# Kernel optimization log

Measured on AMD Instinct MI355X. Metric: run time of the kernel, lower is better.

The kernel has to match this reference:

```python
import jax, jax.numpy as jnp
import numpy as np

N_ELEC = 8192   # electrons (nodes)
N_NUC = 512     # nuclei
EMB = 256       # embedding_dim
KER = 256       # kernel_dim
DF = 64         # dist_feat_dim
MID = 128       # round(sqrt(DF*KER)), log-interpolated hidden width of w-MLP
E = 131072      # edges per edge type


def _ssp(x):
    # shifted softplus, deepqmc default activation: log(0.5*exp(x) + 0.5)
    return jax.nn.softplus(x) - jnp.log(2.0)


def setup_inputs() -> dict:
    key = jax.random.key(0)
    ks = jax.random.split(key, 24)
    def nrm(k, shape, scale):
        return jax.random.normal(k, shape, dtype=jnp.float32) * scale
    inp = {}
    inp['electrons'] = nrm(ks[0], (N_ELEC, EMB), 1.0)
    inp['nuclei'] = nrm(ks[1], (N_NUC, KER), 1.0)
    for i, lbl in enumerate(['same', 'anti', 'n']):
        inp[f'dist_{lbl}'] = jax.random.uniform(ks[2 + i], (E, DF), dtype=jnp.float32)
        inp[f'w1_{lbl}'] = nrm(ks[5 + i], (DF, MID), DF ** -0.5)
        inp[f'b1_{lbl}'] = jnp.zeros((MID,), jnp.float32)
        inp[f'w2_{lbl}'] = nrm(ks[8 + i], (MID, KER), MID ** -0.5)
        inp[f'g_{lbl}'] = nrm(ks[11 + i], (KER, EMB), KER ** -0.5)
    inp['h_w'] = nrm(ks[14], (EMB, KER), EMB ** -0.5)
    inp['senders_same'] = jax.random.randint(ks[15], (E,), 0, N_ELEC)
    inp['senders_anti'] = jax.random.randint(ks[16], (E,), 0, N_ELEC)
    inp['senders_n'] = jax.random.randint(ks[17], (E,), 0, N_NUC)
    inp['receivers_same'] = jax.random.randint(ks[18], (E,), 0, N_ELEC)
    inp['receivers_anti'] = jax.random.randint(ks[19], (E,), 0, N_ELEC)
    inp['receivers_n'] = jax.random.randint(ks[20], (E,), 0, N_ELEC)
    return inp


def reference(electrons, nuclei, dist_same, dist_anti, dist_n,
              w1_same, b1_same, w2_same, w1_anti, b1_anti, w2_anti,
              w1_n, b1_n, w2_n, g_same, g_anti, g_n, h_w,
              senders_same, senders_anti, senders_n,
              receivers_same, receivers_anti, receivers_n):
    def w_mlp(d, w1, b1, w2):
        # MLP with ('log', 2) hidden layers: linear+bias -> SSP -> last linear (no bias)
        return _ssp(d @ w1 + b1) @ w2

    # per-edge filters from distance features: [E, KER]
    we_same = w_mlp(dist_same, w1_same, b1_same, w2_same)
    we_anti = w_mlp(dist_anti, w1_anti, b1_anti, w2_anti)
    we_n = w_mlp(dist_n, w1_n, b1_n, w2_n)

    # shared h (single bias-free linear) on gathered sender electrons: [E, KER]
    hx_same = electrons[senders_same] @ h_w
    hx_anti = electrons[senders_anti] @ h_w

    weh_same = we_same * hx_same
    weh_anti = we_anti * hx_anti
    weh_n = we_n * nuclei[senders_n]

    # scatter-sum messages to receiver electrons: [N_ELEC, KER]
    z_same = jax.ops.segment_sum(weh_same, receivers_same, num_segments=N_ELEC)
    z_anti = jax.ops.segment_sum(weh_anti, receivers_anti, num_segments=N_ELEC)
    z_n = jax.ops.segment_sum(weh_n, receivers_n, num_segments=N_ELEC)

    # per-label g (single bias-free linear) + residual update, order matches original
    return electrons + (z_n @ g_n + z_same @ g_same + z_anti @ g_anti)
```

## Files before the change

kernel.cpp:

```cpp
#include <hip/hip_runtime.h>
#include <stdint.h>


#define N_ELEC 8192
#define N_NUC  512
#define EMB    256
#define KER    256
#define DF     64
#define MID    128
#define NEDGE  131072
#define RPS    8256
#define CSTR   272

using u16 = unsigned short;
typedef short short8 __attribute__((ext_vector_type(8)));
typedef float f32x4 __attribute__((ext_vector_type(4)));

__device__ __forceinline__ float bf2f(u16 h) {
  return __uint_as_float(((unsigned)h) << 16);
}
__device__ __forceinline__ u16 f2bf(float f) {
  unsigned u = __float_as_uint(f);
  return (u16)((u + 0x7FFFu + ((u >> 16) & 1u)) >> 16);
}
__device__ __forceinline__ unsigned pkbf(float a, float b) {
  return ((unsigned)f2bf(b) << 16) | (unsigned)f2bf(a);
}
__device__ __forceinline__ float ssp_fast(float x) {
  const float e = __expf(-fabsf(x));
  return fmaxf(x, 0.f) + __logf(fmaf(0.5f, e, 0.5f));
}

__device__ __forceinline__ void bar_lds() {
  __builtin_amdgcn_sched_barrier(0);
  asm volatile("s_waitcnt lgkmcnt(0)" ::: "memory");
  __builtin_amdgcn_s_barrier();
  __builtin_amdgcn_sched_barrier(0);
}

__device__ __forceinline__ void stage_t64(const char* g0, long stride,
                                          char* lds, int tid) {
  const int l = tid & 63, w = tid >> 6;
  const int r = w * 16 + (l >> 2);
  const int cb = (l & 3) * 16;
  __builtin_amdgcn_global_load_lds(
      (const __attribute__((address_space(1))) unsigned*)(g0 +
                                                          (long)r * stride +
                                                          cb),
      (__attribute__((address_space(3))) unsigned*)(lds + w * 1024), 16, 0, 0);
}
__device__ __forceinline__ void stage_f64(const float* g0, int stride_e,
                                          int kt, char* lds, int tid) {
#pragma unroll
  for (int k = 0; k < 4; ++k) {
    const int idx2 = k * 256 + tid;
    const int row = idx2 >> 4, cp = idx2 & 15;
    const float2 v = *(const float2*)(g0 + (long)row * stride_e + kt + cp * 2);
    *(unsigned*)(lds + row * 64 + cp * 4) = pkbf(v.x, v.y);
  }
}
template <bool A_F32>
__device__ __forceinline__ void gemm64(const char* A0, long as_bytes,
                                       const float* Af, int as_elems,
                                       const char* B0, long bs, int K,
                                       char* As, char* Bs, f32x4 acc[2][2],
                                       int tid) {
  const int l = tid & 63, lane15 = l & 15, quad = l >> 4, wv = tid >> 6;
  const int mw = (wv >> 1) * 32, nw = (wv & 1) * 32;
  for (int kt = 0; kt < K; kt += 32) {
    if (A_F32)
      stage_f64(Af, as_elems, kt, As, tid);
    else
      stage_t64(A0 + (long)kt * 2, as_bytes, As, tid);
    stage_t64(B0 + (long)kt * 2, bs, Bs, tid);
    __syncthreads();
    short8 af[2], bf[2];
#pragma unroll
    for (int i = 0; i < 2; ++i) {
      af[i] = *(const short8*)(As + (mw + i * 16 + lane15) * 64 + quad * 16);
      bf[i] = *(const short8*)(Bs + (nw + i * 16 + lane15) * 64 + quad * 16);
    }
#pragma unroll
    for (int mi = 0; mi < 2; ++mi)
#pragma unroll
      for (int ni = 0; ni < 2; ++ni)
        acc[mi][ni] = __builtin_amdgcn_mfma_f32_16x16x32_bf16(
            af[mi], bf[ni], acc[mi][ni], 0, 0, 0);
    __syncthreads();
  }
}

__global__ __launch_bounds__(256) void k_setup(
    const float* h_w, const float* w1s, const float* w1a, const float* w1n,
    const float* w2s, const float* w2a, const float* w2n, const float* gs,
    const float* ga, const float* gn, u16* hwT, u16* w1T, u16* w2T, u16* gT,
    float4* z, int* cnt) {
  const int b = blockIdx.x;
  if (b < 6144) {
    z[b * 256 + threadIdx.x] = (float4){0.f, 0.f, 0.f, 0.f};
    return;
  }
  if (b < 6240) {
    cnt[(b - 6144) * 256 + threadIdx.x] = 0;
    return;
  }
  int i = (b - 6240) * 256 + threadIdx.x;
  if (i < 65536) {
    int n = i >> 8, k = i & 255;
    hwT[i] = f2bf(h_w[k * 256 + n]);
    return;
  }
  int j = i - 65536;
  if (j < 24576) {
    int t = j >> 13, jj = j & 8191, n = jj >> 6, k = jj & 63;
    const float* w1 = t == 0 ? w1s : (t == 1 ? w1a : w1n);
    w1T[j] = f2bf(w1[k * 128 + n]);
    return;
  }
  j -= 24576;
  if (j < 98304) {
    int t = j >> 15, jj = j & 32767, n = jj >> 7, k = jj & 127;
    const float* w2 = t == 0 ? w2s : (t == 1 ? w2a : w2n);
    w2T[j] = f2bf(w2[k * 256 + n]);
    return;
  }
  j -= 98304;
  if (j < 196608) {
    int n = j / 768, q = j % 768, t = q >> 8, k = q & 255;
    const float* g = t == 0 ? gs : (t == 1 ? ga : gn);
    gT[j] = f2bf(g[k * 256 + n]);
  }
}

__global__ __launch_bounds__(256) void k_hist(const int* r0, const int* r1,
                                              const int* r2, int* cnt) {
  const int t = blockIdx.z;
  const int* rcv = t == 0 ? r0 : (t == 1 ? r1 : r2);
  const int e = blockIdx.x * 256 + threadIdx.x;
  atomicAdd(&cnt[t * N_ELEC + rcv[e]], 1);
}

__global__ __launch_bounds__(256) void k_scan(const int* cnt, int* rowptr,
                                              int* cursor) {
  const int t = blockIdx.x, tid = threadIdx.x;
  __shared__ int part[256];
  const int* c = cnt + t * N_ELEC;
  int s = 0;
#pragma unroll
  for (int i = 0; i < 32; ++i) s += c[tid * 32 + i];
  part[tid] = s;
  __syncthreads();
  for (int off = 1; off < 256; off <<= 1) {
    int v = (tid >= off) ? part[tid - off] : 0;
    __syncthreads();
    part[tid] += v;
    __syncthreads();
  }
  int run = (tid == 0) ? 0 : part[tid - 1];
  int* rp = rowptr + t * RPS;
  int* cu = cursor + t * N_ELEC;
  for (int i = 0; i < 32; ++i) {
    rp[tid * 32 + i] = run;
    cu[tid * 32 + i] = run;
    run += c[tid * 32 + i];
  }
  if (tid == 255) rp[N_ELEC] = run;
}

__global__ __launch_bounds__(256) void k_place(const int* r0, const int* r1,
                                               const int* r2, const int* s0,
                                               const int* s1, const int* s2,
                                               int* cursor, int* perm,
                                               int* snd_s, int* rcv_s) {
  const int t = blockIdx.z;
  const int* rcv = t == 0 ? r0 : (t == 1 ? r1 : r2);
  const int* snd = t == 0 ? s0 : (t == 1 ? s1 : s2);
  const int e = blockIdx.x * 256 + threadIdx.x;
  const int rr = rcv[e];
  const int pos = atomicAdd(&cursor[t * N_ELEC + rr], 1);
  perm[t * NEDGE + pos] = e;
  snd_s[t * NEDGE + pos] = snd[e];
  rcv_s[t * NEDGE + pos] = rr;
}

__global__ __launch_bounds__(256) void k_he(const float* elec, const u16* hwT,
                                            u16* he) {
  __shared__ char As[4096], Bs[4096];
  f32x4 acc[2][2];
#pragma unroll
  for (int i = 0; i < 2; ++i)
#pragma unroll
    for (int j = 0; j < 2; ++j) acc[i][j] = (f32x4){0.f, 0.f, 0.f, 0.f};
  const int m0 = blockIdx.x * 64, n0 = blockIdx.y * 64;
  gemm64<true>(nullptr, 0, elec + (long)m0 * 256, 256,
               (const char*)hwT + (long)n0 * 512, 512, 256, As, Bs, acc,
               threadIdx.x);
  const int l = threadIdx.x & 63, lane15 = l & 15, quad = l >> 4,
            wv = threadIdx.x >> 6;
  const int mw = (wv >> 1) * 32, nw = (wv & 1) * 32;
#pragma unroll
  for (int mi = 0; mi < 2; ++mi)
#pragma unroll
    for (int r = 0; r < 4; ++r) {
      const int row = m0 + mw + mi * 16 + quad * 4 + r;
#pragma unroll
      for (int ni = 0; ni < 2; ++ni) {
        const int col = n0 + nw + ni * 16 + lane15;
        he[row * 256 + col] = f2bf(acc[mi][ni][r]);
      }
    }
}

__global__ __launch_bounds__(256, 3) void k_edge(
    const float* d0, const float* d1, const float* d2, const float* b0,
    const float* b1p, const float* b2, const u16* w1T, const u16* w2T,
    const u16* he, const float* nucf, const int* perm, const int* snd_s,
    const int* rcv_s, float* z) {
  __shared__ char mid[128 * CSTR];
  __shared__ char hc[64 * CSTR];
  __shared__ int snd_l[128], rcv_l[128];

  const int t = blockIdx.z;
  const int m0 = blockIdx.x * 128;
  const int tid = threadIdx.x;
  const float* dist = t == 0 ? d0 : (t == 1 ? d1 : d2);
  const float* bias = t == 0 ? b0 : (t == 1 ? b1p : b2);
  const u16* w1t = w1T + t * 8192;
  const u16* w2t = w2T + t * 32768;
  const bool is_nuc = (t == 2);

  if (tid < 128)
    snd_l[tid] = snd_s[t * NEDGE + m0 + tid];
  else
    rcv_l[tid - 128] = rcv_s[t * NEDGE + m0 + tid - 128];

  int rows[4];
  const int* pm = perm + t * NEDGE + m0;
#pragma unroll
  for (int s = 0; s < 4; ++s) rows[s] = pm[(s * 256 + tid) >> 3];
#pragma unroll
  for (int j = 0; j < 2; ++j)
#pragma unroll
    for (int s = 0; s < 4; ++s) {
      const int idx = s * 256 + tid, row = idx >> 3, ch = idx & 7;
      const float4 v =
          *(const float4*)(dist + (long)rows[s] * 64 + j * 32 + ch * 4);
      uint2 p;
      p.x = pkbf(v.x, v.y);
      p.y = pkbf(v.z, v.w);
      *(uint2*)(mid + j * 8192 + row * 64 + ch * 8) = p;
    }
  bar_lds();

  const int l = tid & 63, lane15 = l & 15, quad = l >> 4, wv = tid >> 6;
  const int mw = (wv >> 1) * 64, nw = (wv & 1) * 64;

  f32x4 acc[4][4];
#pragma unroll
  for (int i = 0; i < 4; ++i)
#pragma unroll
    for (int j = 0; j < 4; ++j) acc[i][j] = (f32x4){0.f, 0.f, 0.f, 0.f};
#pragma unroll
  for (int j = 0; j < 2; ++j) {
    short8 af[4], bf[4];
#pragma unroll
    for (int i = 0; i < 4; ++i) {
      af[i] = *(const short8*)(mid + j * 8192 + (mw + i * 16 + lane15) * 64 +
                               quad * 16);
      bf[i] = *(const short8*)(w1t + (nw + i * 16 + lane15) * 64 + j * 32 +
                               quad * 8);
    }
#pragma unroll
    for (int mi = 0; mi < 4; ++mi)
#pragma unroll
      for (int ni = 0; ni < 4; ++ni)
        acc[mi][ni] = __builtin_amdgcn_mfma_f32_16x16x32_bf16(
            af[mi], bf[ni], acc[mi][ni], 0, 0, 0);
  }
  bar_lds();

#pragma unroll
  for (int mi = 0; mi < 4; ++mi)
#pragma unroll
    for (int r = 0; r < 4; ++r) {
      const int row = mw + mi * 16 + quad * 4 + r;
#pragma unroll
      for (int ni = 0; ni < 4; ++ni) {
        const int col = nw + ni * 16 + lane15;
        const float x = acc[mi][ni][r] + bias[col];
        *(u16*)(mid + row * CSTR + col * 2) = f2bf(ssp_fast(x));
      }
    }
  bar_lds();

  for (int n0 = 0; n0 < 256; n0 += 128) {
#pragma unroll
    for (int i = 0; i < 4; ++i)
#pragma unroll
      for (int j = 0; j < 4; ++j) acc[i][j] = (f32x4){0.f, 0.f, 0.f, 0.f};
#pragma unroll
    for (int kt = 0; kt < 128; kt += 32) {
      short8 af[4], bf[4];
#pragma unroll
      for (int i = 0; i < 4; ++i) {
        af[i] = *(const short8*)(mid + (mw + i * 16 + lane15) * CSTR + kt * 2 +
                                 quad * 16);
        bf[i] = *(const short8*)(w2t + (n0 + nw + i * 16 + lane15) * 128 + kt +
                                 quad * 8);
      }
#pragma unroll
      for (int mi = 0; mi < 4; ++mi)
#pragma unroll
        for (int ni = 0; ni < 4; ++ni)
          acc[mi][ni] = __builtin_amdgcn_mfma_f32_16x16x32_bf16(
              af[mi], bf[ni], acc[mi][ni], 0, 0, 0);
    }

    for (int h = 0; h < 2; ++h) {
      const int rbase = h * 64;
      if (!is_nuc) {
#pragma unroll
        for (int c = 0; c < 4; ++c) {
          const int chunk = c * 256 + tid;
          const int row = chunk >> 4, off = chunk & 15;
          const uint4 v =
              *(const uint4*)((const char*)he +
                              (size_t)snd_l[rbase + row] * 512 + n0 * 2 +
                              off * 16);
          *(uint4*)(hc + row * CSTR + off * 16) = v;
        }
      } else {
#pragma unroll
        for (int c = 0; c < 4; ++c) {
          const int chunk = c * 256 + tid;
          const int row = chunk >> 4, off = chunk & 15;
          const char* src = (const char*)nucf +
                            (size_t)snd_l[rbase + row] * 1024 + n0 * 4 +
                            off * 32;
          const float4 a = *(const float4*)src;
          const float4 b = *(const float4*)(src + 16);
          uint4 p;
          p.x = pkbf(a.x, a.y);
          p.y = pkbf(a.z, a.w);
          p.z = pkbf(b.x, b.y);
          p.w = pkbf(b.z, b.w);
          *(uint4*)(hc + row * CSTR + off * 16) = p;
        }
      }
      bar_lds();

      if ((wv >> 1) == h) {
#pragma unroll
        for (int mi = 0; mi < 4; ++mi)
#pragma unroll
          for (int r = 0; r < 4; ++r) {
            const int lrow = mi * 16 + quad * 4 + r;
#pragma unroll
            for (int ni = 0; ni < 4; ++ni) {
              const int col = nw + ni * 16 + lane15;
              u16* p = (u16*)(hc + lrow * CSTR) + col;
              *p = f2bf(acc[mi][ni][r] * bf2f(*p));
            }
          }
      }
      bar_lds();

      {
        const int cp = l;
        const int rbeg = wv * 16, rend = rbeg + 16;
        float a0 = 0.f, a1 = 0.f;
        int cur = rcv_l[rbase + rbeg];
        for (int row = rbeg; row < rend; ++row) {
          const unsigned p = *(const unsigned*)(hc + row * CSTR + cp * 4);
          a0 += __uint_as_float(p << 16);
          a1 += __uint_as_float(p & 0xffff0000u);
          const int nxt = (row + 1 < rend) ? rcv_l[rbase + row + 1] : -1;
          if (nxt != cur) {
            float* zp = z + (size_t)cur * 768 + t * 256 + n0 + cp * 2;
            unsafeAtomicAdd(zp, a0);
            unsafeAtomicAdd(zp + 1, a1);
            a0 = a1 = 0.f;
            cur = nxt;
          }
        }
      }
      bar_lds();
    }
  }
}

__global__ __launch_bounds__(256) void k_final(const float* z, const u16* gT,
                                               const float* elec, float* out) {
  __shared__ char As[4096], Bs[4096];
  f32x4 acc[2][2];
#pragma unroll
  for (int i = 0; i < 2; ++i)
#pragma unroll
    for (int j = 0; j < 2; ++j) acc[i][j] = (f32x4){0.f, 0.f, 0.f, 0.f};
  const int m0 = blockIdx.x * 64, n0 = blockIdx.y * 64;
  gemm64<true>(nullptr, 0, z + (long)m0 * 768, 768,
               (const char*)gT + (long)n0 * 1536, 1536, 768, As, Bs, acc,
               threadIdx.x);
  const int l = threadIdx.x & 63, lane15 = l & 15, quad = l >> 4,
            wv = threadIdx.x >> 6;
  const int mw = (wv >> 1) * 32, nw = (wv & 1) * 32;
#pragma unroll
  for (int mi = 0; mi < 2; ++mi)
#pragma unroll
    for (int r = 0; r < 4; ++r) {
      const int row = m0 + mw + mi * 16 + quad * 4 + r;
#pragma unroll
      for (int ni = 0; ni < 2; ++ni) {
        const int col = n0 + nw + ni * 16 + lane15;
        out[row * 256 + col] = acc[mi][ni][r] + elec[row * 256 + col];
      }
    }
}

extern "C" void kernel_launch(void* const* d_in, const int* in_sizes, int n_in,
                              void* d_out, int out_size, void* d_ws,
                              size_t ws_size, hipStream_t stream) {
  int I_dist[3], I_w1[3], I_b1[3], I_w2[3], I_g[3], I_hw;
  if (in_sizes[3] == 64 * 128) {
    for (int t = 0; t < 3; ++t) {
      I_dist[t] = 2 + t * 5 + 0;
      I_w1[t] = 2 + t * 5 + 1;
      I_b1[t] = 2 + t * 5 + 2;
      I_w2[t] = 2 + t * 5 + 3;
      I_g[t] = 2 + t * 5 + 4;
    }
    I_hw = 17;
  } else {
    I_dist[0] = 2; I_dist[1] = 3; I_dist[2] = 4;
    I_w1[0] = 5;  I_b1[0] = 6;  I_w2[0] = 7;
    I_w1[1] = 8;  I_b1[1] = 9;  I_w2[1] = 10;
    I_w1[2] = 11; I_b1[2] = 12; I_w2[2] = 13;
    I_g[0] = 14; I_g[1] = 15; I_g[2] = 16;
    I_hw = 17;
  }
  const int I_snd[3] = {18, 19, 20};
  const int I_rcv[3] = {21, 22, 23};

  char* ws = (char*)d_ws;
  u16* he = (u16*)(ws + 0);
  u16* hwT = (u16*)(ws + 4194304);
  u16* w1T = (u16*)(ws + 4325376);
  u16* w2T = (u16*)(ws + 4374528);
  u16* gT = (u16*)(ws + 4571136);
  float* z = (float*)(ws + 4964352);
  int* cnt = (int*)(ws + 30130176);
  int* rowptr = (int*)(ws + 30228480);
  int* cursor = (int*)(ws + 30327552);
  int* perm = (int*)(ws + 30425856);
  int* snd_s = (int*)(ws + 31998720);
  int* rcv_s = (int*)(ws + 33571584);

  const float* elec = (const float*)d_in[0];
  const float* nuc = (const float*)d_in[1];
  const int* s0 = (const int*)d_in[I_snd[0]];
  const int* s1 = (const int*)d_in[I_snd[1]];
  const int* s2 = (const int*)d_in[I_snd[2]];
  const int* r0 = (const int*)d_in[I_rcv[0]];
  const int* r1 = (const int*)d_in[I_rcv[1]];
  const int* r2 = (const int*)d_in[I_rcv[2]];

  k_setup<<<7744, 256, 0, stream>>>(
      (const float*)d_in[I_hw], (const float*)d_in[I_w1[0]],
      (const float*)d_in[I_w1[1]], (const float*)d_in[I_w1[2]],
      (const float*)d_in[I_w2[0]], (const float*)d_in[I_w2[1]],
      (const float*)d_in[I_w2[2]], (const float*)d_in[I_g[0]],
      (const float*)d_in[I_g[1]], (const float*)d_in[I_g[2]], hwT, w1T, w2T,
      gT, (float4*)z, cnt);

  k_hist<<<dim3(NEDGE / 256, 1, 3), 256, 0, stream>>>(r0, r1, r2, cnt);
  k_scan<<<3, 256, 0, stream>>>(cnt, rowptr, cursor);
  k_place<<<dim3(NEDGE / 256, 1, 3), 256, 0, stream>>>(r0, r1, r2, s0, s1, s2,
                                                       cursor, perm, snd_s,
                                                       rcv_s);

  k_he<<<dim3(N_ELEC / 64, 4), 256, 0, stream>>>(elec, hwT, he);

  k_edge<<<dim3(NEDGE / 128, 1, 3), 256, 0, stream>>>(
      (const float*)d_in[I_dist[0]], (const float*)d_in[I_dist[1]],
      (const float*)d_in[I_dist[2]], (const float*)d_in[I_b1[0]],
      (const float*)d_in[I_b1[1]], (const float*)d_in[I_b1[2]], w1T, w2T, he,
      nuc, perm, snd_s, rcv_s, z);

  k_final<<<dim3(N_ELEC / 64, 4), 256, 0, stream>>>(z, gT, elec,
                                                    (float*)d_out);
}
```

Measured before the change: 403.4 us.

## Pack sorted edge metadata into u64 and double k_edge threads to 512

```diff
diff --git a/kernel.cpp b/kernel.cpp
--- a/kernel.cpp
+++ b/kernel.cpp
@@ -13,6 +13,7 @@
 #define CSTR   272
 
 using u16 = unsigned short;
+using u64 = unsigned long long;
 typedef short short8 __attribute__((ext_vector_type(8)));
 typedef float f32x4 __attribute__((ext_vector_type(4)));
 
@@ -170,17 +171,15 @@
 __global__ __launch_bounds__(256) void k_place(const int* r0, const int* r1,
                                                const int* r2, const int* s0,
                                                const int* s1, const int* s2,
-                                               int* cursor, int* perm,
-                                               int* snd_s, int* rcv_s) {
+                                               int* cursor, u64* pk) {
   const int t = blockIdx.z;
   const int* rcv = t == 0 ? r0 : (t == 1 ? r1 : r2);
   const int* snd = t == 0 ? s0 : (t == 1 ? s1 : s2);
   const int e = blockIdx.x * 256 + threadIdx.x;
   const int rr = rcv[e];
   const int pos = atomicAdd(&cursor[t * N_ELEC + rr], 1);
-  perm[t * NEDGE + pos] = e;
-  snd_s[t * NEDGE + pos] = snd[e];
-  rcv_s[t * NEDGE + pos] = rr;
+  pk[t * NEDGE + pos] =
+      (u64)(unsigned)e | ((u64)(unsigned)snd[e] << 17) | ((u64)(unsigned)rr << 30);
 }
 
 __global__ __launch_bounds__(256) void k_he(const float* elec, const u16* hwT,
@@ -211,11 +210,10 @@
     }
 }
 
-__global__ __launch_bounds__(256, 3) void k_edge(
+__global__ __launch_bounds__(512, 6) void k_edge(
     const float* d0, const float* d1, const float* d2, const float* b0,
     const float* b1p, const float* b2, const u16* w1T, const u16* w2T,
-    const u16* he, const float* nucf, const int* perm, const int* snd_s,
-    const int* rcv_s, float* z) {
+    const u16* he, const float* nucf, const u64* pk, float* z) {
   __shared__ char mid[128 * CSTR];
   __shared__ char hc[64 * CSTR];
   __shared__ int snd_l[128], rcv_l[128];
@@ -228,21 +226,23 @@
   const u16* w1t = w1T + t * 8192;
   const u16* w2t = w2T + t * 32768;
   const bool is_nuc = (t == 2);
-
-  if (tid < 128)
-    snd_l[tid] = snd_s[t * NEDGE + m0 + tid];
-  else
-    rcv_l[tid - 128] = rcv_s[t * NEDGE + m0 + tid - 128];
-
-  int rows[4];
-  const int* pm = perm + t * NEDGE + m0;
-#pragma unroll
-  for (int s = 0; s < 4; ++s) rows[s] = pm[(s * 256 + tid) >> 3];
+  const u64* pkt = pk + (size_t)t * NEDGE + m0;
+
+  if (tid < 128) {
+    const u64 rec = pkt[tid];
+    snd_l[tid] = (int)((rec >> 17) & 0x1FFFu);
+    rcv_l[tid] = (int)(rec >> 30);
+  }
+
+  int rows[2];
+#pragma unroll
+  for (int s = 0; s < 2; ++s)
+    rows[s] = (int)(pkt[(s * 512 + tid) >> 3] & 0x1FFFFu);
 #pragma unroll
   for (int j = 0; j < 2; ++j)
 #pragma unroll
-    for (int s = 0; s < 4; ++s) {
-      const int idx = s * 256 + tid, row = idx >> 3, ch = idx & 7;
+    for (int s = 0; s < 2; ++s) {
+      const int idx = s * 512 + tid, row = idx >> 3, ch = idx & 7;
       const float4 v =
           *(const float4*)(dist + (long)rows[s] * 64 + j * 32 + ch * 4);
       uint2 p;
@@ -253,27 +253,30 @@
   bar_lds();
 
   const int l = tid & 63, lane15 = l & 15, quad = l >> 4, wv = tid >> 6;
-  const int mw = (wv >> 1) * 64, nw = (wv & 1) * 64;
-
-  f32x4 acc[4][4];
+  const int mwh = wv >> 2;
+  const int mw = mwh * 64;
+  const int nw = (wv & 3) * 32;
+
+  f32x4 acc[4][2];
 #pragma unroll
   for (int i = 0; i < 4; ++i)
 #pragma unroll
-    for (int j = 0; j < 4; ++j) acc[i][j] = (f32x4){0.f, 0.f, 0.f, 0.f};
+    for (int j = 0; j < 2; ++j) acc[i][j] = (f32x4){0.f, 0.f, 0.f, 0.f};
 #pragma unroll
   for (int j = 0; j < 2; ++j) {
-    short8 af[4], bf[4];
-#pragma unroll
-    for (int i = 0; i < 4; ++i) {
+    short8 af[4], bf[2];
+#pragma unroll
+    for (int i = 0; i < 4; ++i)
       af[i] = *(const short8*)(mid + j * 8192 + (mw + i * 16 + lane15) * 64 +
                                quad * 16);
+#pragma unroll
+    for (int i = 0; i < 2; ++i)
       bf[i] = *(const short8*)(w1t + (nw + i * 16 + lane15) * 64 + j * 32 +
                                quad * 8);
-    }
 #pragma unroll
     for (int mi = 0; mi < 4; ++mi)
 #pragma unroll
-      for (int ni = 0; ni < 4; ++ni)
+      for (int ni = 0; ni < 2; ++ni)
         acc[mi][ni] = __builtin_amdgcn_mfma_f32_16x16x32_bf16(
             af[mi], bf[ni], acc[mi][ni], 0, 0, 0);
   }
@@ -285,7 +288,7 @@
     for (int r = 0; r < 4; ++r) {
       const int row = mw + mi * 16 + quad * 4 + r;
 #pragma unroll
-      for (int ni = 0; ni < 4; ++ni) {
+      for (int ni = 0; ni < 2; ++ni) {
         const int col = nw + ni * 16 + lane15;
         const float x = acc[mi][ni][r] + bias[col];
         *(u16*)(mid + row * CSTR + col * 2) = f2bf(ssp_fast(x));
@@ -297,21 +300,22 @@
 #pragma unroll
     for (int i = 0; i < 4; ++i)
 #pragma unroll
-      for (int j = 0; j < 4; ++j) acc[i][j] = (f32x4){0.f, 0.f, 0.f, 0.f};
+      for (int j = 0; j < 2; ++j) acc[i][j] = (f32x4){0.f, 0.f, 0.f, 0.f};
 #pragma unroll
     for (int kt = 0; kt < 128; kt += 32) {
-      short8 af[4], bf[4];
-#pragma unroll
-      for (int i = 0; i < 4; ++i) {
+      short8 af[4], bf[2];
+#pragma unroll
+      for (int i = 0; i < 4; ++i)
         af[i] = *(const short8*)(mid + (mw + i * 16 + lane15) * CSTR + kt * 2 +
                                  quad * 16);
+#pragma unroll
+      for (int i = 0; i < 2; ++i)
         bf[i] = *(const short8*)(w2t + (n0 + nw + i * 16 + lane15) * 128 + kt +
                                  quad * 8);
-      }
 #pragma unroll
       for (int mi = 0; mi < 4; ++mi)
 #pragma unroll
-        for (int ni = 0; ni < 4; ++ni)
+        for (int ni = 0; ni < 2; ++ni)
           acc[mi][ni] = __builtin_amdgcn_mfma_f32_16x16x32_bf16(
               af[mi], bf[ni], acc[mi][ni], 0, 0, 0);
     }
@@ -320,8 +324,8 @@
       const int rbase = h * 64;
       if (!is_nuc) {
 #pragma unroll
-        for (int c = 0; c < 4; ++c) {
-          const int chunk = c * 256 + tid;
+        for (int c = 0; c < 2; ++c) {
+          const int chunk = c * 512 + tid;
           const int row = chunk >> 4, off = chunk & 15;
           const uint4 v =
               *(const uint4*)((const char*)he +
@@ -331,8 +335,8 @@
         }
       } else {
 #pragma unroll
-        for (int c = 0; c < 4; ++c) {
-          const int chunk = c * 256 + tid;
+        for (int c = 0; c < 2; ++c) {
+          const int chunk = c * 512 + tid;
           const int row = chunk >> 4, off = chunk & 15;
           const char* src = (const char*)nucf +
                             (size_t)snd_l[rbase + row] * 1024 + n0 * 4 +
@@ -349,14 +353,14 @@
       }
       bar_lds();
 
-      if ((wv >> 1) == h) {
+      if (mwh == h) {
 #pragma unroll
         for (int mi = 0; mi < 4; ++mi)
 #pragma unroll
           for (int r = 0; r < 4; ++r) {
             const int lrow = mi * 16 + quad * 4 + r;
 #pragma unroll
-            for (int ni = 0; ni < 4; ++ni) {
+            for (int ni = 0; ni < 2; ++ni) {
               const int col = nw + ni * 16 + lane15;
               u16* p = (u16*)(hc + lrow * CSTR) + col;
               *p = f2bf(acc[mi][ni][r] * bf2f(*p));
@@ -367,7 +371,7 @@
 
       {
         const int cp = l;
-        const int rbeg = wv * 16, rend = rbeg + 16;
+        const int rbeg = wv * 8, rend = rbeg + 8;
         float a0 = 0.f, a1 = 0.f;
         int cur = rcv_l[rbase + rbeg];
         for (int row = rbeg; row < rend; ++row) {
@@ -451,9 +455,7 @@
   int* cnt = (int*)(ws + 30130176);
   int* rowptr = (int*)(ws + 30228480);
   int* cursor = (int*)(ws + 30327552);
-  int* perm = (int*)(ws + 30425856);
-  int* snd_s = (int*)(ws + 31998720);
-  int* rcv_s = (int*)(ws + 33571584);
+  u64* pk = (u64*)(ws + 30425856);
 
   const float* elec = (const float*)d_in[0];
   const float* nuc = (const float*)d_in[1];
@@ -475,16 +477,15 @@
   k_hist<<<dim3(NEDGE / 256, 1, 3), 256, 0, stream>>>(r0, r1, r2, cnt);
   k_scan<<<3, 256, 0, stream>>>(cnt, rowptr, cursor);
   k_place<<<dim3(NEDGE / 256, 1, 3), 256, 0, stream>>>(r0, r1, r2, s0, s1, s2,
-                                                       cursor, perm, snd_s,
-                                                       rcv_s);
+                                                       cursor, pk);
 
   k_he<<<dim3(N_ELEC / 64, 4), 256, 0, stream>>>(elec, hwT, he);
 
-  k_edge<<<dim3(NEDGE / 128, 1, 3), 256, 0, stream>>>(
+  k_edge<<<dim3(NEDGE / 128, 1, 3), 512, 0, stream>>>(
       (const float*)d_in[I_dist[0]], (const float*)d_in[I_dist[1]],
       (const float*)d_in[I_dist[2]], (const float*)d_in[I_b1[0]],
       (const float*)d_in[I_b1[1]], (const float*)d_in[I_b1[2]], w1T, w2T, he,
-      nuc, perm, snd_s, rcv_s, z);
+      nuc, pk, z);
 
   k_final<<<dim3(N_ELEC / 64, 4), 256, 0, stream>>>(z, gT, elec,
                                                     (float*)d_out);
```

New measurement: 421.3 us. 1.04x slower.

## Accumulate per-receiver segments in LDS slots and pack edge indices into u64

Applied to the files above, without the earlier changes.

```diff
diff --git a/kernel.cpp b/kernel.cpp
--- a/kernel.cpp
+++ b/kernel.cpp
@@ -11,8 +11,10 @@
 #define NEDGE  131072
 #define RPS    8256
 #define CSTR   272
+#define NSLOT  16
 
 using u16 = unsigned short;
+using u64 = unsigned long long;
 typedef short short8 __attribute__((ext_vector_type(8)));
 typedef float f32x4 __attribute__((ext_vector_type(4)));
 
@@ -170,17 +172,15 @@
 __global__ __launch_bounds__(256) void k_place(const int* r0, const int* r1,
                                                const int* r2, const int* s0,
                                                const int* s1, const int* s2,
-                                               int* cursor, int* perm,
-                                               int* snd_s, int* rcv_s) {
+                                               int* cursor, u64* pk) {
   const int t = blockIdx.z;
   const int* rcv = t == 0 ? r0 : (t == 1 ? r1 : r2);
   const int* snd = t == 0 ? s0 : (t == 1 ? s1 : s2);
   const int e = blockIdx.x * 256 + threadIdx.x;
   const int rr = rcv[e];
   const int pos = atomicAdd(&cursor[t * N_ELEC + rr], 1);
-  perm[t * NEDGE + pos] = e;
-  snd_s[t * NEDGE + pos] = snd[e];
-  rcv_s[t * NEDGE + pos] = rr;
+  pk[t * NEDGE + pos] =
+      (u64)(unsigned)e | ((u64)(unsigned)snd[e] << 17) | ((u64)(unsigned)rr << 30);
 }
 
 __global__ __launch_bounds__(256) void k_he(const float* elec, const u16* hwT,
@@ -214,11 +214,13 @@
 __global__ __launch_bounds__(256, 3) void k_edge(
     const float* d0, const float* d1, const float* d2, const float* b0,
     const float* b1p, const float* b2, const u16* w1T, const u16* w2T,
-    const u16* he, const float* nucf, const int* perm, const int* snd_s,
-    const int* rcv_s, float* z) {
+    const u16* he, const float* nucf, const u64* pk, float* z) {
   __shared__ char mid[128 * CSTR];
-  __shared__ char hc[64 * CSTR];
-  __shared__ int snd_l[128], rcv_l[128];
+  __shared__ char hc[32 * CSTR];
+  __shared__ float zacc[NSLOT][128];
+  __shared__ int snd_l[128], rcv_l[128], slot_l[128];
+  __shared__ int rcv_slot[NSLOT];
+  __shared__ int cnt_w[2], nslots_s;
 
   const int t = blockIdx.z;
   const int m0 = blockIdx.x * 128;
@@ -228,16 +230,22 @@
   const u16* w1t = w1T + t * 8192;
   const u16* w2t = w2T + t * 32768;
   const bool is_nuc = (t == 2);
-
-  if (tid < 128)
-    snd_l[tid] = snd_s[t * NEDGE + m0 + tid];
-  else
-    rcv_l[tid - 128] = rcv_s[t * NEDGE + m0 + tid - 128];
-
+  const u64* pkt = pk + (size_t)t * NEDGE + m0;
+
+  if (tid < 128) {
+    const u64 rec = pkt[tid];
+    snd_l[tid] = (int)((rec >> 17) & 0x1FFFu);
+    rcv_l[tid] = (int)(rec >> 30);
+  }
+  {
+    float* zf = &zacc[0][0];
+#pragma unroll
+    for (int i = 0; i < 8; ++i) zf[i * 256 + tid] = 0.f;
+  }
   int rows[4];
-  const int* pm = perm + t * NEDGE + m0;
-#pragma unroll
-  for (int s = 0; s < 4; ++s) rows[s] = pm[(s * 256 + tid) >> 3];
+#pragma unroll
+  for (int s = 0; s < 4; ++s)
+    rows[s] = (int)(pkt[(s * 256 + tid) >> 3] & 0x1FFFFu);
 #pragma unroll
   for (int j = 0; j < 2; ++j)
 #pragma unroll
@@ -252,6 +260,25 @@
     }
   bar_lds();
 
+  {
+    bool flag = false;
+    int pre = 0;
+    if (tid < 128) {
+      const int rcv = rcv_l[tid];
+      flag = (tid > 0) && (rcv != rcv_l[tid - 1]);
+      const u64 m = __ballot(flag);
+      pre = (int)__popcll(m & ((1ull << (tid & 63)) - 1ull));
+      if ((tid & 63) == 0) cnt_w[tid >> 6] = (int)__popcll(m);
+    }
+    bar_lds();
+    if (tid < 128) {
+      const int slot = pre + (flag ? 1 : 0) + ((tid >= 64) ? cnt_w[0] : 0);
+      slot_l[tid] = slot;
+      if ((flag || tid == 0) && slot < NSLOT) rcv_slot[slot] = rcv_l[tid];
+      if (tid == 0) nslots_s = cnt_w[0] + cnt_w[1] + 1;
+    }
+  }
+
   const int l = tid & 63, lane15 = l & 15, quad = l >> 4, wv = tid >> 6;
   const int mw = (wv >> 1) * 64, nw = (wv & 1) * 64;
 
@@ -316,11 +343,11 @@
               af[mi], bf[ni], acc[mi][ni], 0, 0, 0);
     }
 
-    for (int h = 0; h < 2; ++h) {
-      const int rbase = h * 64;
+    for (int q = 0; q < 4; ++q) {
+      const int rbase = q * 32;
       if (!is_nuc) {
 #pragma unroll
-        for (int c = 0; c < 4; ++c) {
+        for (int c = 0; c < 2; ++c) {
           const int chunk = c * 256 + tid;
           const int row = chunk >> 4, off = chunk & 15;
           const uint4 v =
@@ -331,7 +358,7 @@
         }
       } else {
 #pragma unroll
-        for (int c = 0; c < 4; ++c) {
+        for (int c = 0; c < 2; ++c) {
           const int chunk = c * 256 + tid;
           const int row = chunk >> 4, off = chunk & 15;
           const char* src = (const char*)nucf +
@@ -349,12 +376,14 @@
       }
       bar_lds();
 
-      if ((wv >> 1) == h) {
-#pragma unroll
-        for (int mi = 0; mi < 4; ++mi)
+      if ((wv >> 1) == (q >> 1)) {
+        const int mi0 = (q & 1) * 2;
+#pragma unroll
+        for (int mi2 = 0; mi2 < 2; ++mi2) {
+          const int mi = mi0 + mi2;
 #pragma unroll
           for (int r = 0; r < 4; ++r) {
-            const int lrow = mi * 16 + quad * 4 + r;
+            const int lrow = mi2 * 16 + quad * 4 + r;
 #pragma unroll
             for (int ni = 0; ni < 4; ++ni) {
               const int col = nw + ni * 16 + lane15;
@@ -362,29 +391,60 @@
               *p = f2bf(acc[mi][ni][r] * bf2f(*p));
             }
           }
+        }
       }
       bar_lds();
 
       {
         const int cp = l;
-        const int rbeg = wv * 16, rend = rbeg + 16;
+        const int lr0 = wv * 8;
         float a0 = 0.f, a1 = 0.f;
-        int cur = rcv_l[rbase + rbeg];
-        for (int row = rbeg; row < rend; ++row) {
-          const unsigned p = *(const unsigned*)(hc + row * CSTR + cp * 4);
+        int cs = slot_l[rbase + lr0];
+        for (int i = 0; i < 8; ++i) {
+          const int lr = lr0 + i, gr = rbase + lr;
+          const unsigned p = *(const unsigned*)(hc + lr * CSTR + cp * 4);
           a0 += __uint_as_float(p << 16);
           a1 += __uint_as_float(p & 0xffff0000u);
-          const int nxt = (row + 1 < rend) ? rcv_l[rbase + row + 1] : -1;
-          if (nxt != cur) {
-            float* zp = z + (size_t)cur * 768 + t * 256 + n0 + cp * 2;
-            unsafeAtomicAdd(zp, a0);
-            unsafeAtomicAdd(zp + 1, a1);
+          const int ns = (i + 1 < 8) ? slot_l[gr + 1] : -1;
+          if (ns != cs) {
+            if (cs < NSLOT) {
+              atomicAdd(&zacc[cs][cp * 2], a0);
+              atomicAdd(&zacc[cs][cp * 2 + 1], a1);
+            } else {
+              float* zp =
+                  z + (size_t)rcv_l[gr] * 768 + t * 256 + n0 + cp * 2;
+              unsafeAtomicAdd(zp, a0);
+              unsafeAtomicAdd(zp + 1, a1);
+            }
             a0 = a1 = 0.f;
-            cur = nxt;
+            cs = ns;
           }
         }
       }
       bar_lds();
+    }
+
+    {
+      const int nsl = nslots_s;
+      const int s = tid >> 4, c0 = (tid & 15) * 8;
+      if (s < nsl && s < NSLOT) {
+        const int r = rcv_slot[s];
+        float* zp = z + (size_t)r * 768 + t * 256 + n0 + c0;
+        if (s == 0 || s == nsl - 1) {
+#pragma unroll
+          for (int jj = 0; jj < 8; ++jj)
+            unsafeAtomicAdd(zp + jj, zacc[s][c0 + jj]);
+        } else {
+          *(float4*)zp = *(float4*)&zacc[s][c0];
+          *(float4*)(zp + 4) = *(float4*)&zacc[s][c0 + 4];
+        }
+      }
+    }
+    bar_lds();
+    {
+      float* zf = &zacc[0][0];
+#pragma unroll
+      for (int i = 0; i < 8; ++i) zf[i * 256 + tid] = 0.f;
     }
   }
 }
@@ -451,9 +511,7 @@
   int* cnt = (int*)(ws + 30130176);
   int* rowptr = (int*)(ws + 30228480);
   int* cursor = (int*)(ws + 30327552);
-  int* perm = (int*)(ws + 30425856);
-  int* snd_s = (int*)(ws + 31998720);
-  int* rcv_s = (int*)(ws + 33571584);
+  u64* pk = (u64*)(ws + 30425856);
 
   const float* elec = (const float*)d_in[0];
   const float* nuc = (const float*)d_in[1];
@@ -475,8 +533,7 @@
   k_hist<<<dim3(NEDGE / 256, 1, 3), 256, 0, stream>>>(r0, r1, r2, cnt);
   k_scan<<<3, 256, 0, stream>>>(cnt, rowptr, cursor);
   k_place<<<dim3(NEDGE / 256, 1, 3), 256, 0, stream>>>(r0, r1, r2, s0, s1, s2,
-                                                       cursor, perm, snd_s,
-                                                       rcv_s);
+                                                       cursor, pk);
 
   k_he<<<dim3(N_ELEC / 64, 4), 256, 0, stream>>>(elec, hwT, he);
 
@@ -484,7 +541,7 @@
       (const float*)d_in[I_dist[0]], (const float*)d_in[I_dist[1]],
       (const float*)d_in[I_dist[2]], (const float*)d_in[I_b1[0]],
       (const float*)d_in[I_b1[1]], (const float*)d_in[I_b1[2]], w1T, w2T, he,
-      nuc, perm, snd_s, rcv_s, z);
+      nuc, pk, z);
 
   k_final<<<dim3(N_ELEC / 64, 4), 256, 0, stream>>>(z, gT, elec,
                                                     (float*)d_out);
```

After: 570.0 us. 1.41x slower.

## Pack edge sort records into u64 and retile dense GEMMs to full-width rows

Applied to the files above, without the earlier changes.

```diff
diff --git a/kernel.cpp b/kernel.cpp
--- a/kernel.cpp
+++ b/kernel.cpp
@@ -13,6 +13,7 @@
 #define CSTR   272
 
 using u16 = unsigned short;
+using u64 = unsigned long long;
 typedef short short8 __attribute__((ext_vector_type(8)));
 typedef float f32x4 __attribute__((ext_vector_type(4)));
 
@@ -38,55 +39,14 @@
   __builtin_amdgcn_sched_barrier(0);
 }
 
-__device__ __forceinline__ void stage_t64(const char* g0, long stride,
-                                          char* lds, int tid) {
-  const int l = tid & 63, w = tid >> 6;
-  const int r = w * 16 + (l >> 2);
-  const int cb = (l & 3) * 16;
-  __builtin_amdgcn_global_load_lds(
-      (const __attribute__((address_space(1))) unsigned*)(g0 +
-                                                          (long)r * stride +
-                                                          cb),
-      (__attribute__((address_space(3))) unsigned*)(lds + w * 1024), 16, 0, 0);
-}
-__device__ __forceinline__ void stage_f64(const float* g0, int stride_e,
-                                          int kt, char* lds, int tid) {
-#pragma unroll
-  for (int k = 0; k < 4; ++k) {
+__device__ __forceinline__ void stage_f32x32(const float* g0, int stride_e,
+                                             int kt, char* lds, int tid) {
+#pragma unroll
+  for (int k = 0; k < 2; ++k) {
     const int idx2 = k * 256 + tid;
     const int row = idx2 >> 4, cp = idx2 & 15;
     const float2 v = *(const float2*)(g0 + (long)row * stride_e + kt + cp * 2);
     *(unsigned*)(lds + row * 64 + cp * 4) = pkbf(v.x, v.y);
-  }
-}
-template <bool A_F32>
-__device__ __forceinline__ void gemm64(const char* A0, long as_bytes,
-                                       const float* Af, int as_elems,
-                                       const char* B0, long bs, int K,
-                                       char* As, char* Bs, f32x4 acc[2][2],
-                                       int tid) {
-  const int l = tid & 63, lane15 = l & 15, quad = l >> 4, wv = tid >> 6;
-  const int mw = (wv >> 1) * 32, nw = (wv & 1) * 32;
-  for (int kt = 0; kt < K; kt += 32) {
-    if (A_F32)
-      stage_f64(Af, as_elems, kt, As, tid);
-    else
-      stage_t64(A0 + (long)kt * 2, as_bytes, As, tid);
-    stage_t64(B0 + (long)kt * 2, bs, Bs, tid);
-    __syncthreads();
-    short8 af[2], bf[2];
-#pragma unroll
-    for (int i = 0; i < 2; ++i) {
-      af[i] = *(const short8*)(As + (mw + i * 16 + lane15) * 64 + quad * 16);
-      bf[i] = *(const short8*)(Bs + (nw + i * 16 + lane15) * 64 + quad * 16);
-    }
-#pragma unroll
-    for (int mi = 0; mi < 2; ++mi)
-#pragma unroll
-      for (int ni = 0; ni < 2; ++ni)
-        acc[mi][ni] = __builtin_amdgcn_mfma_f32_16x16x32_bf16(
-            af[mi], bf[ni], acc[mi][ni], 0, 0, 0);
-    __syncthreads();
   }
 }
 
@@ -170,42 +130,56 @@
 __global__ __launch_bounds__(256) void k_place(const int* r0, const int* r1,
                                                const int* r2, const int* s0,
                                                const int* s1, const int* s2,
-                                               int* cursor, int* perm,
-                                               int* snd_s, int* rcv_s) {
+                                               int* cursor, u64* pk) {
   const int t = blockIdx.z;
   const int* rcv = t == 0 ? r0 : (t == 1 ? r1 : r2);
   const int* snd = t == 0 ? s0 : (t == 1 ? s1 : s2);
   const int e = blockIdx.x * 256 + threadIdx.x;
   const int rr = rcv[e];
   const int pos = atomicAdd(&cursor[t * N_ELEC + rr], 1);
-  perm[t * NEDGE + pos] = e;
-  snd_s[t * NEDGE + pos] = snd[e];
-  rcv_s[t * NEDGE + pos] = rr;
+  pk[t * NEDGE + pos] =
+      (u64)(unsigned)e | ((u64)(unsigned)snd[e] << 17) | ((u64)(unsigned)rr << 30);
 }
 
 __global__ __launch_bounds__(256) void k_he(const float* elec, const u16* hwT,
                                             u16* he) {
-  __shared__ char As[4096], Bs[4096];
-  f32x4 acc[2][2];
+  __shared__ __align__(16) char As[2048];
+  const int tid = threadIdx.x;
+  const int m0 = blockIdx.x * 32;
+  const int l = tid & 63, lane15 = l & 15, quad = l >> 4, wv = tid >> 6;
+  const int nw = wv * 64;
+  f32x4 acc[2][4];
 #pragma unroll
   for (int i = 0; i < 2; ++i)
 #pragma unroll
-    for (int j = 0; j < 2; ++j) acc[i][j] = (f32x4){0.f, 0.f, 0.f, 0.f};
-  const int m0 = blockIdx.x * 64, n0 = blockIdx.y * 64;
-  gemm64<true>(nullptr, 0, elec + (long)m0 * 256, 256,
-               (const char*)hwT + (long)n0 * 512, 512, 256, As, Bs, acc,
-               threadIdx.x);
-  const int l = threadIdx.x & 63, lane15 = l & 15, quad = l >> 4,
-            wv = threadIdx.x >> 6;
-  const int mw = (wv >> 1) * 32, nw = (wv & 1) * 32;
+    for (int j = 0; j < 4; ++j) acc[i][j] = (f32x4){0.f, 0.f, 0.f, 0.f};
+  for (int kt = 0; kt < 256; kt += 32) {
+    stage_f32x32(elec + (long)m0 * 256, 256, kt, As, tid);
+    __syncthreads();
+    short8 af[2], bf[4];
+#pragma unroll
+    for (int i = 0; i < 2; ++i)
+      af[i] = *(const short8*)(As + (i * 16 + lane15) * 64 + quad * 16);
+#pragma unroll
+    for (int i = 0; i < 4; ++i)
+      bf[i] = *(const short8*)(hwT + (nw + i * 16 + lane15) * 256 + kt +
+                               quad * 8);
+#pragma unroll
+    for (int mi = 0; mi < 2; ++mi)
+#pragma unroll
+      for (int ni = 0; ni < 4; ++ni)
+        acc[mi][ni] = __builtin_amdgcn_mfma_f32_16x16x32_bf16(
+            af[mi], bf[ni], acc[mi][ni], 0, 0, 0);
+    __syncthreads();
+  }
 #pragma unroll
   for (int mi = 0; mi < 2; ++mi)
 #pragma unroll
     for (int r = 0; r < 4; ++r) {
-      const int row = m0 + mw + mi * 16 + quad * 4 + r;
-#pragma unroll
-      for (int ni = 0; ni < 2; ++ni) {
-        const int col = n0 + nw + ni * 16 + lane15;
+      const int row = m0 + mi * 16 + quad * 4 + r;
+#pragma unroll
+      for (int ni = 0; ni < 4; ++ni) {
+        const int col = nw + ni * 16 + lane15;
         he[row * 256 + col] = f2bf(acc[mi][ni][r]);
       }
     }
@@ -214,8 +188,7 @@
 __global__ __launch_bounds__(256, 3) void k_edge(
     const float* d0, const float* d1, const float* d2, const float* b0,
     const float* b1p, const float* b2, const u16* w1T, const u16* w2T,
-    const u16* he, const float* nucf, const int* perm, const int* snd_s,
-    const int* rcv_s, float* z) {
+    const u16* he, const float* nucf, const u64* pk, float* z) {
   __shared__ char mid[128 * CSTR];
   __shared__ char hc[64 * CSTR];
   __shared__ int snd_l[128], rcv_l[128];
@@ -228,16 +201,18 @@
   const u16* w1t = w1T + t * 8192;
   const u16* w2t = w2T + t * 32768;
   const bool is_nuc = (t == 2);
-
-  if (tid < 128)
-    snd_l[tid] = snd_s[t * NEDGE + m0 + tid];
-  else
-    rcv_l[tid - 128] = rcv_s[t * NEDGE + m0 + tid - 128];
+  const u64* pkt = pk + (size_t)t * NEDGE + m0;
+
+  if (tid < 128) {
+    const u64 rec = pkt[tid];
+    snd_l[tid] = (int)((rec >> 17) & 0x1FFFu);
+    rcv_l[tid] = (int)(rec >> 30);
+  }
 
   int rows[4];
-  const int* pm = perm + t * NEDGE + m0;
-#pragma unroll
-  for (int s = 0; s < 4; ++s) rows[s] = pm[(s * 256 + tid) >> 3];
+#pragma unroll
+  for (int s = 0; s < 4; ++s)
+    rows[s] = (int)(pkt[(s * 256 + tid) >> 3] & 0x1FFFFu);
 #pragma unroll
   for (int j = 0; j < 2; ++j)
 #pragma unroll
@@ -391,27 +366,43 @@
 
 __global__ __launch_bounds__(256) void k_final(const float* z, const u16* gT,
                                                const float* elec, float* out) {
-  __shared__ char As[4096], Bs[4096];
-  f32x4 acc[2][2];
+  __shared__ __align__(16) char As[2048];
+  const int tid = threadIdx.x;
+  const int m0 = blockIdx.x * 32;
+  const int l = tid & 63, lane15 = l & 15, quad = l >> 4, wv = tid >> 6;
+  const int nw = wv * 64;
+  f32x4 acc[2][4];
 #pragma unroll
   for (int i = 0; i < 2; ++i)
 #pragma unroll
-    for (int j = 0; j < 2; ++j) acc[i][j] = (f32x4){0.f, 0.f, 0.f, 0.f};
-  const int m0 = blockIdx.x * 64, n0 = blockIdx.y * 64;
-  gemm64<true>(nullptr, 0, z + (long)m0 * 768, 768,
-               (const char*)gT + (long)n0 * 1536, 1536, 768, As, Bs, acc,
-               threadIdx.x);
-  const int l = threadIdx.x & 63, lane15 = l & 15, quad = l >> 4,
-            wv = threadIdx.x >> 6;
-  const int mw = (wv >> 1) * 32, nw = (wv & 1) * 32;
+    for (int j = 0; j < 4; ++j) acc[i][j] = (f32x4){0.f, 0.f, 0.f, 0.f};
+  for (int kt = 0; kt < 768; kt += 32) {
+    stage_f32x32(z + (long)m0 * 768, 768, kt, As, tid);
+    __syncthreads();
+    short8 af[2], bf[4];
+#pragma unroll
+    for (int i = 0; i < 2; ++i)
+      af[i] = *(const short8*)(As + (i * 16 + lane15) * 64 + quad * 16);
+#pragma unroll
+    for (int i = 0; i < 4; ++i)
+      bf[i] = *(const short8*)(gT + (nw + i * 16 + lane15) * 768 + kt +
+                               quad * 8);
+#pragma unroll
+    for (int mi = 0; mi < 2; ++mi)
+#pragma unroll
+      for (int ni = 0; ni < 4; ++ni)
+        acc[mi][ni] = __builtin_amdgcn_mfma_f32_16x16x32_bf16(
+            af[mi], bf[ni], acc[mi][ni], 0, 0, 0);
+    __syncthreads();
+  }
 #pragma unroll
   for (int mi = 0; mi < 2; ++mi)
 #pragma unroll
     for (int r = 0; r < 4; ++r) {
-      const int row = m0 + mw + mi * 16 + quad * 4 + r;
-#pragma unroll
-      for (int ni = 0; ni < 2; ++ni) {
-        const int col = n0 + nw + ni * 16 + lane15;
+      const int row = m0 + mi * 16 + quad * 4 + r;
+#pragma unroll
+      for (int ni = 0; ni < 4; ++ni) {
+        const int col = nw + ni * 16 + lane15;
         out[row * 256 + col] = acc[mi][ni][r] + elec[row * 256 + col];
       }
     }
@@ -451,9 +442,7 @@
   int* cnt = (int*)(ws + 30130176);
   int* rowptr = (int*)(ws + 30228480);
   int* cursor = (int*)(ws + 30327552);
-  int* perm = (int*)(ws + 30425856);
-  int* snd_s = (int*)(ws + 31998720);
-  int* rcv_s = (int*)(ws + 33571584);
+  u64* pk = (u64*)(ws + 30425856);
 
   const float* elec = (const float*)d_in[0];
   const float* nuc = (const float*)d_in[1];
@@ -475,17 +464,15 @@
   k_hist<<<dim3(NEDGE / 256, 1, 3), 256, 0, stream>>>(r0, r1, r2, cnt);
   k_scan<<<3, 256, 0, stream>>>(cnt, rowptr, cursor);
   k_place<<<dim3(NEDGE / 256, 1, 3), 256, 0, stream>>>(r0, r1, r2, s0, s1, s2,
-                                                       cursor, perm, snd_s,
-                                                       rcv_s);
-
-  k_he<<<dim3(N_ELEC / 64, 4), 256, 0, stream>>>(elec, hwT, he);
+                                                       cursor, pk);
+
+  k_he<<<N_ELEC / 32, 256, 0, stream>>>(elec, hwT, he);
 
   k_edge<<<dim3(NEDGE / 128, 1, 3), 256, 0, stream>>>(
       (const float*)d_in[I_dist[0]], (const float*)d_in[I_dist[1]],
       (const float*)d_in[I_dist[2]], (const float*)d_in[I_b1[0]],
       (const float*)d_in[I_b1[1]], (const float*)d_in[I_b1[2]], w1T, w2T, he,
-      nuc, perm, snd_s, rcv_s, z);
-
-  k_final<<<dim3(N_ELEC / 64, 4), 256, 0, stream>>>(z, gT, elec,
-                                                    (float*)d_out);
-}
+      nuc, pk, z);
+
+  k_final<<<N_ELEC / 32, 256, 0, stream>>>(z, gT, elec, (float*)d_out);
+}
```

After: 401.0 us. About the same (-0.6%).
